# Performance work log

Hardware: AMD Instinct MI355X
Metric: run time of the kernel (lower is better)

## Reference

```python
import jax, jax.numpy as jnp
import numpy as np

INPUT_SIZE = 2048
H1 = 256
H2 = 64
NB = 8
BATCH = 16384


def setup_inputs() -> dict:
    key = jax.random.key(0)
    ks = jax.random.split(key, 8)
    x = jax.random.normal(ks[0], (BATCH, INPUT_SIZE), dtype=jnp.float32)
    bucket_indices = jax.random.randint(ks[1], (BATCH,), 0, NB, dtype=jnp.int32)
    # torch nn.Linear weights: (out_features, in_features), bias: (out_features,)
    def lin(k, fan_in, fan_out):
        kw, kb = jax.random.split(k)
        bound = 1.0 / np.sqrt(fan_in)
        W = jax.random.uniform(kw, (fan_out, fan_in), jnp.float32, -bound, bound)
        b = jax.random.uniform(kb, (fan_out,), jnp.float32, -bound, bound)
        return W, b
    W1, b1 = lin(ks[2], INPUT_SIZE, H1 * NB)
    W2, b2 = lin(ks[3], H1, H2 * NB)
    W3, b3 = lin(ks[4], H2, 1 * NB)
    return {"x": x, "bucket_indices": bucket_indices,
            "W1": W1, "b1": b1, "W2": W2, "b2": b2, "W3": W3, "b3": b3}


def _gather_bucket(all_out, idx, width):
    # all_out: (B, NB*width) -> select per-sample bucket slice -> (B, width)
    B = all_out.shape[0]
    per = all_out.reshape(B, NB, width)
    return jnp.take_along_axis(per, idx[:, None, None], axis=1)[:, 0, :]


def reference(x, bucket_indices, W1, b1, W2, b2, W3, b3):
    idx = bucket_indices.astype(jnp.int32)
    h1_all = x @ W1.T + b1                      # (B, H1*NB)
    h1 = jnp.clip(_gather_bucket(h1_all, idx, H1), 0.0, 1.0)
    h2_all = h1 @ W2.T + b2                     # (B, H2*NB)
    h2 = jnp.clip(_gather_bucket(h2_all, idx, H2), 0.0, 1.0)
    out_all = h2 @ W3.T + b3                    # (B, NB)
    out = _gather_bucket(out_all, idx, 1)       # (B, 1)
    return out[:, :, None]                      # (B, 1, 1) matches unsqueeze(-1)
```

## Files before the change

### kernel.cpp

```cpp
#include <hip/hip_runtime.h>

#define INSZ   2048
#define NH1    256
#define NH2    64
#define NB     8
#define BATCH  16384

#define TS        32
#define MAXTILES  (BATCH / TS)
#define GRIDX     (NB * MAXTILES)

#define W1F_U4   (NB * 64 * 16 * 64)
#define W2F_U4   (NB * 8 * 4 * 64)

#define META_OFF  0
#define ORDER_OFF 1024
#define W1F_OFF   (1024 + BATCH * 4)
#define W2F_OFF   (W1F_OFF + W1F_U4 * 16)
#define WS_NEED   (W2F_OFF + W2F_U4 * 16)

typedef float f4  __attribute__((ext_vector_type(4)));
typedef float f32x4 __attribute__((ext_vector_type(4)));
typedef short bf16x8 __attribute__((ext_vector_type(8)));

__device__ __forceinline__ unsigned short f2bf(float f) {
    unsigned u = __float_as_uint(f);
    u += 0x7fffu + ((u >> 16) & 1u);
    return (unsigned short)(u >> 16);
}
__device__ __forceinline__ float clamp01(float v) { return fminf(fmaxf(v, 0.0f), 1.0f); }
__device__ __forceinline__ unsigned pack2(float a, float b) {
    return (unsigned)f2bf(a) | ((unsigned)f2bf(b) << 16);
}
__device__ __forceinline__ bf16x8 mk8(uint2 lo, uint2 hi) {
    union { unsigned u[4]; bf16x8 v; } r;
    r.u[0] = lo.x; r.u[1] = lo.y; r.u[2] = hi.x; r.u[3] = hi.y;
    return r.v;
}


__global__ void k_countscan(const int* __restrict__ idx, int* __restrict__ meta) {
    __shared__ int scnt[NB];
    int t = threadIdx.x;
    if (t < NB) scnt[t] = 0;
    __syncthreads();
    int local[NB];
#pragma unroll
    for (int bb = 0; bb < NB; bb++) local[bb] = 0;
    for (int i = t; i < BATCH; i += 1024) {
        int b = idx[i];
#pragma unroll
        for (int bb = 0; bb < NB; bb++) local[bb] += (b == bb) ? 1 : 0;
    }
#pragma unroll
    for (int bb = 0; bb < NB; bb++) {
        int v = local[bb];
        v += __shfl_xor(v, 1);  v += __shfl_xor(v, 2);  v += __shfl_xor(v, 4);
        v += __shfl_xor(v, 8);  v += __shfl_xor(v, 16); v += __shfl_xor(v, 32);
        if ((t & 63) == 0) atomicAdd(&scnt[bb], v);
    }
    __syncthreads();
    if (t == 0) {
        int run = 0;
        for (int b = 0; b < NB; b++) {
            int c = scnt[b];
            meta[b]      = c;
            meta[8 + b]  = run;
            meta[16 + b] = run;
            run += c;
        }
    }
}

__global__ void k_scatter(const int* __restrict__ idx, int* __restrict__ meta,
                          int* __restrict__ order) {
    __shared__ int wcnt[16][NB];
    __shared__ int sbase[NB];
    int t = threadIdx.x;
    int i = blockIdx.x * 1024 + t;
    int b = idx[i];
    int wv = t >> 6, lane = t & 63;
    unsigned long long mymask = 0;
#pragma unroll
    for (int bb = 0; bb < NB; bb++) {
        unsigned long long m = __ballot(b == bb);
        if (b == bb) mymask = m;
        if (lane == bb) wcnt[wv][bb] = (int)__popcll(m);
    }
    int myrank = (int)__popcll(mymask & ((1ull << lane) - 1ull));
    __syncthreads();
    if (t < NB) {
        int sum = 0;
        for (int w2 = 0; w2 < 16; w2++) { int c = wcnt[w2][t]; wcnt[w2][t] = sum; sum += c; }
        sbase[t] = atomicAdd(&meta[16 + t], sum);
    }
    __syncthreads();
    order[sbase[b] + wcnt[wv][b] + myrank] = i;
}

__global__ void k_pack(const float* __restrict__ W1, const float* __restrict__ W2,
                       uint4* __restrict__ W1f, uint4* __restrict__ W2f) {
    int u = blockIdx.x * 256 + threadIdx.x;
    if (u < W1F_U4) {
        int k8 = u & 255, row = (u >> 8) & 255, bkt = u >> 16;
        int kb = k8 >> 2, quad = k8 & 3;
        int cb = row >> 4, l15 = row & 15;
        const float* p = W1 + ((size_t)(bkt * NH1 + row)) * INSZ + k8 * 8;
        f4 lo = *(const f4*)p, hi = *(const f4*)(p + 4);
        uint4 o;
        o.x = pack2(lo[0], lo[1]); o.y = pack2(lo[2], lo[3]);
        o.z = pack2(hi[0], hi[1]); o.w = pack2(hi[2], hi[3]);
        W1f[((bkt * 64 + kb) * 16 + cb) * 64 + quad * 16 + l15] = o;
    } else {
        int v = u - W1F_U4;
        if (v >= W2F_U4) return;
        int k8 = v & 31, row = (v >> 5) & 63, bkt = v >> 11;
        int kb2 = k8 >> 2, quad = k8 & 3;
        int cg2 = row >> 4, l15 = row & 15;
        const float* p = W2 + ((size_t)(bkt * NH2 + row)) * NH1 + k8 * 8;
        f4 lo = *(const f4*)p, hi = *(const f4*)(p + 4);
        uint4 o;
        o.x = pack2(lo[0], lo[1]); o.y = pack2(lo[2], lo[3]);
        o.z = pack2(hi[0], hi[1]); o.w = pack2(hi[2], hi[3]);
        W2f[((bkt * 8 + kb2) * 4 + cg2) * 64 + quad * 16 + l15] = o;
    }
}


#define MFMA16 __builtin_amdgcn_mfma_f32_16x16x32_bf16

__global__ __launch_bounds__(512, 2) void fused_v13(
    const float* __restrict__ x, const int* __restrict__ meta,
    const int* __restrict__ order,
    const short* __restrict__ W1f, const short* __restrict__ W2f,
    const float* __restrict__ b1, const float* __restrict__ b2,
    const float* __restrict__ W3, const float* __restrict__ b3,
    float* __restrict__ out)
{
    const int bkt  = blockIdx.x & 7;
    const int tile = blockIdx.x >> 3;
    const int cnt  = meta[bkt];
    const int base = tile * TS;
    if (base >= cnt) return;
    const int off = meta[8 + bkt];

    __shared__ short sX[16 * 1152];
    __shared__ short sh1[TS * 264];
    __shared__ float sPart[4][TS];

    const int t = threadIdx.x;
    const int lane = t & 63, w = t >> 6;
    const int l15 = lane & 15, quad = lane >> 4;

    const int xr = t >> 4, c16 = t & 15;
    int ir = base + xr; if (ir > cnt - 1) ir = cnt - 1;
    const float* xrow = x + (size_t)order[off + ir] * INSZ;

    const short* wp = W1f + ((size_t)bkt << 19) + (size_t)(2 * w) * 512 + lane * 8;

    f32x4 acc[2][2];
#pragma unroll
    for (int f = 0; f < 2; f++)
#pragma unroll
        for (int j = 0; j < 2; j++) acc[f][j] = (f32x4)0.0f;

#pragma unroll 1
    for (int s = 0; s < 4; s++) {
        if (s) __syncthreads();
#pragma unroll
        for (int j = 0; j < 8; j++) {
            const int col = s * 512 + c16 * 4 + j * 64;
            f4 v = *(const f4*)(xrow + col);
            const int kbL = (col >> 5) & 15, ko = col & 31;
            uint2 pk; pk.x = pack2(v[0], v[1]); pk.y = pack2(v[2], v[3]);
            *(uint2*)&sX[kbL * 1152 + xr * 36 + ko] = pk;
        }
        __syncthreads();

#pragma unroll
        for (int kbL = 0; kbL < 16; kbL++) {
            const int kb = s * 16 + kbL;
            const int ab = kbL * 1152 + l15 * 36 + quad * 8;
            uint2 lo0 = *(const uint2*)&sX[ab];
            uint2 hi0 = *(const uint2*)&sX[ab + 4];
            uint2 lo1 = *(const uint2*)&sX[ab + 576];
            uint2 hi1 = *(const uint2*)&sX[ab + 580];
            bf16x8 a0 = mk8(lo0, hi0);
            bf16x8 a1 = mk8(lo1, hi1);
            bf16x8 w0 = *(const bf16x8*)(wp + (size_t)kb * 8192);
            bf16x8 w1 = *(const bf16x8*)(wp + (size_t)kb * 8192 + 512);
            acc[0][0] = MFMA16(a0, w0, acc[0][0], 0, 0, 0);
            acc[0][1] = MFMA16(a0, w1, acc[0][1], 0, 0, 0);
            acc[1][0] = MFMA16(a1, w0, acc[1][0], 0, 0, 0);
            acc[1][1] = MFMA16(a1, w1, acc[1][1], 0, 0, 0);
        }
    }

#pragma unroll
    for (int j = 0; j < 2; j++) {
        int col = w * 32 + j * 16 + l15;
        float bias = b1[bkt * NH1 + col];
#pragma unroll
        for (int f = 0; f < 2; f++)
#pragma unroll
            for (int r = 0; r < 4; r++) {
                int row = f * 16 + quad * 4 + r;
                sh1[row * 264 + col] = (short)f2bf(clamp01(acc[f][j][r] + bias));
            }
    }
    __syncthreads();

    const int rw = w & 1, cg2 = w >> 1;
    f32x4 c2 = (f32x4)0.0f;
    const short* w2p = W2f + (size_t)bkt * 16384 + lane * 8;
#pragma unroll
    for (int kb2 = 0; kb2 < 8; kb2++) {
        bf16x8 a2 = *(const bf16x8*)&sh1[(rw * 16 + l15) * 264 + kb2 * 32 + quad * 8];
        bf16x8 bw = *(const bf16x8*)(w2p + (kb2 * 4 + cg2) * 512);
        c2 = MFMA16(a2, bw, c2, 0, 0, 0);
    }

    {
        int n2 = cg2 * 16 + l15;
        float bias2 = b2[bkt * NH2 + n2];
        float w3v   = W3[bkt * NH2 + n2];
        float sacc[4];
#pragma unroll
        for (int r = 0; r < 4; r++)
            sacc[r] = clamp01(c2[r] + bias2) * w3v;
#pragma unroll
        for (int r = 0; r < 4; r++) {
            float pp = sacc[r];
            pp += __shfl_xor(pp, 1); pp += __shfl_xor(pp, 2);
            pp += __shfl_xor(pp, 4); pp += __shfl_xor(pp, 8);
            if (l15 == 0) sPart[cg2][rw * 16 + quad * 4 + r] = pp;
        }
    }
    __syncthreads();
    if (t < TS && base + t < cnt)
        out[order[off + base + t]] =
            sPart[0][t] + sPart[1][t] + sPart[2][t] + sPart[3][t] + b3[bkt];
}


__global__ void naive_mlp(const float* __restrict__ x, const int* __restrict__ idx,
                          const float* __restrict__ W1, const float* __restrict__ b1,
                          const float* __restrict__ W2, const float* __restrict__ b2,
                          const float* __restrict__ W3, const float* __restrict__ b3,
                          float* __restrict__ out)
{
    int i = blockIdx.x;
    int b = idx[i];
    __shared__ float sx[INSZ];
    __shared__ float sh1n[NH1];
    __shared__ float sh2n[NH2];
    for (int t = threadIdx.x; t < INSZ; t += 256) sx[t] = x[(size_t)i * INSZ + t];
    __syncthreads();
    int j = threadIdx.x;
    {
        const float* wr = W1 + (size_t)(b * NH1 + j) * INSZ;
        float acc = b1[b * NH1 + j];
        for (int k = 0; k < INSZ; k++) acc += sx[k] * wr[k];
        sh1n[j] = fminf(fmaxf(acc, 0.f), 1.f);
    }
    __syncthreads();
    if (j < NH2) {
        const float* wr = W2 + (size_t)(b * NH2 + j) * NH1;
        float acc = b2[b * NH2 + j];
        for (int k = 0; k < NH1; k++) acc += sh1n[k] * wr[k];
        sh2n[j] = fminf(fmaxf(acc, 0.f), 1.f);
    }
    __syncthreads();
    if (j == 0) {
        float acc = b3[b];
        for (int k = 0; k < NH2; k++) acc += sh2n[k] * W3[b * NH2 + k];
        out[i] = acc;
    }
}

extern "C" void kernel_launch(void* const* d_in, const int* in_sizes, int n_in,
                              void* d_out, int out_size, void* d_ws, size_t ws_size,
                              hipStream_t stream) {
    const float* x  = (const float*)d_in[0];
    const int* bidx = (const int*)d_in[1];
    const float* W1 = (const float*)d_in[2];
    const float* b1 = (const float*)d_in[3];
    const float* W2 = (const float*)d_in[4];
    const float* b2 = (const float*)d_in[5];
    const float* W3 = (const float*)d_in[6];
    const float* b3 = (const float*)d_in[7];
    float* out = (float*)d_out;

    if (ws_size >= (size_t)WS_NEED) {
        char* ws = (char*)d_ws;
        int*   meta  = (int*)(ws + META_OFF);
        int*   order = (int*)(ws + ORDER_OFF);
        uint4* W1f   = (uint4*)(ws + W1F_OFF);
        uint4* W2f   = (uint4*)(ws + W2F_OFF);

        k_countscan<<<1, 1024, 0, stream>>>(bidx, meta);
        k_scatter<<<BATCH / 1024, 1024, 0, stream>>>(bidx, meta, order);
        k_pack<<<(W1F_U4 + W2F_U4) / 256, 256, 0, stream>>>(W1, W2, W1f, W2f);
        fused_v13<<<GRIDX, 512, 0, stream>>>(x, meta, order,
                                             (const short*)W1f, (const short*)W2f,
                                             b1, b2, W3, b3, out);
    } else {
        naive_mlp<<<BATCH, 256, 0, stream>>>(x, bidx, W1, b1, W2, b2, W3, b3, out);
    }
}
```

Measured before the change: 275.3 us.

## Load x directly into MFMA registers, drop LDS staging, halve row tile

Shrinks the per-block row tile from 32 to 16 samples and the block from 512 to 256 threads. Each lane now reads its x fragment straight from global memory and converts it to bf16 in registers, so the shared-memory staging buffer and its barriers are gone. Each wave now computes 64 hidden columns for all 16 rows instead of 32 columns for 32 rows. The cost is that W1 is reused across only 16 rows, which doubles W1 traffic per sample, and the x reads are less coalesced (8 floats per lane per row).

Measured after the change: 333.0 us. 1.21x slower.

```diff
diff --git a/kernel.cpp b/kernel.cpp
--- a/kernel.cpp
+++ b/kernel.cpp
@@ -6,7 +6,7 @@
 #define NB     8
 #define BATCH  16384
 
-#define TS        32
+#define TS        16
 #define MAXTILES  (BATCH / TS)
 #define GRIDX     (NB * MAXTILES)
 
@@ -31,11 +31,6 @@
 __device__ __forceinline__ float clamp01(float v) { return fminf(fmaxf(v, 0.0f), 1.0f); }
 __device__ __forceinline__ unsigned pack2(float a, float b) {
     return (unsigned)f2bf(a) | ((unsigned)f2bf(b) << 16);
-}
-__device__ __forceinline__ bf16x8 mk8(uint2 lo, uint2 hi) {
-    union { unsigned u[4]; bf16x8 v; } r;
-    r.u[0] = lo.x; r.u[1] = lo.y; r.u[2] = hi.x; r.u[3] = hi.y;
-    return r.v;
 }
 
 
@@ -129,7 +124,7 @@
 
 #define MFMA16 __builtin_amdgcn_mfma_f32_16x16x32_bf16
 
-__global__ __launch_bounds__(512, 2) void fused_v13(
+__global__ __launch_bounds__(256, 4) void fused_v14(
     const float* __restrict__ x, const int* __restrict__ meta,
     const int* __restrict__ order,
     const short* __restrict__ W1f, const short* __restrict__ W2f,
@@ -144,7 +139,6 @@
     if (base >= cnt) return;
     const int off = meta[8 + bkt];
 
-    __shared__ short sX[16 * 1152];
     __shared__ short sh1[TS * 264];
     __shared__ float sPart[4][TS];
 
@@ -152,88 +146,65 @@
     const int lane = t & 63, w = t >> 6;
     const int l15 = lane & 15, quad = lane >> 4;
 
-    const int xr = t >> 4, c16 = t & 15;
-    int ir = base + xr; if (ir > cnt - 1) ir = cnt - 1;
-    const float* xrow = x + (size_t)order[off + ir] * INSZ;
-
-    const short* wp = W1f + ((size_t)bkt << 19) + (size_t)(2 * w) * 512 + lane * 8;
-
-    f32x4 acc[2][2];
-#pragma unroll
-    for (int f = 0; f < 2; f++)
-#pragma unroll
-        for (int j = 0; j < 2; j++) acc[f][j] = (f32x4)0.0f;
-
-#pragma unroll 1
-    for (int s = 0; s < 4; s++) {
-        if (s) __syncthreads();
-#pragma unroll
-        for (int j = 0; j < 8; j++) {
-            const int col = s * 512 + c16 * 4 + j * 64;
-            f4 v = *(const f4*)(xrow + col);
-            const int kbL = (col >> 5) & 15, ko = col & 31;
-            uint2 pk; pk.x = pack2(v[0], v[1]); pk.y = pack2(v[2], v[3]);
-            *(uint2*)&sX[kbL * 1152 + xr * 36 + ko] = pk;
+    int ir = base + l15; if (ir > cnt - 1) ir = cnt - 1;
+    const float* xg = x + (size_t)order[off + ir] * INSZ + quad * 8;
+
+    const short* wp = W1f + ((size_t)bkt << 19) + (size_t)(4 * w) * 512 + lane * 8;
+
+    f32x4 acc[4];
+#pragma unroll
+    for (int i = 0; i < 4; i++) acc[i] = (f32x4)0.0f;
+
+#pragma unroll 2
+    for (int kb = 0; kb < 64; kb++) {
+        f4 lo = *(const f4*)(xg + kb * 32);
+        f4 hi = *(const f4*)(xg + kb * 32 + 4);
+        const short* wq = wp + (size_t)kb * 8192;
+        bf16x8 w0 = *(const bf16x8*)(wq);
+        bf16x8 w1 = *(const bf16x8*)(wq + 512);
+        bf16x8 w2 = *(const bf16x8*)(wq + 1024);
+        bf16x8 w3r = *(const bf16x8*)(wq + 1536);
+        uint4 u;
+        u.x = pack2(lo[0], lo[1]); u.y = pack2(lo[2], lo[3]);
+        u.z = pack2(hi[0], hi[1]); u.w = pack2(hi[2], hi[3]);
+        bf16x8 a = *(bf16x8*)&u;
+        acc[0] = MFMA16(a, w0, acc[0], 0, 0, 0);
+        acc[1] = MFMA16(a, w1, acc[1], 0, 0, 0);
+        acc[2] = MFMA16(a, w2, acc[2], 0, 0, 0);
+        acc[3] = MFMA16(a, w3r, acc[3], 0, 0, 0);
+    }
+
+#pragma unroll
+    for (int i = 0; i < 4; i++) {
+        int col = w * 64 + i * 16 + l15;
+        float bias = b1[bkt * NH1 + col];
+#pragma unroll
+        for (int r = 0; r < 4; r++) {
+            int row = quad * 4 + r;
+            sh1[row * 264 + col] = (short)f2bf(clamp01(acc[i][r] + bias));
         }
-        __syncthreads();
-
-#pragma unroll
-        for (int kbL = 0; kbL < 16; kbL++) {
-            const int kb = s * 16 + kbL;
-            const int ab = kbL * 1152 + l15 * 36 + quad * 8;
-            uint2 lo0 = *(const uint2*)&sX[ab];
-            uint2 hi0 = *(const uint2*)&sX[ab + 4];
-            uint2 lo1 = *(const uint2*)&sX[ab + 576];
-            uint2 hi1 = *(const uint2*)&sX[ab + 580];
-            bf16x8 a0 = mk8(lo0, hi0);
-            bf16x8 a1 = mk8(lo1, hi1);
-            bf16x8 w0 = *(const bf16x8*)(wp + (size_t)kb * 8192);
-            bf16x8 w1 = *(const bf16x8*)(wp + (size_t)kb * 8192 + 512);
-            acc[0][0] = MFMA16(a0, w0, acc[0][0], 0, 0, 0);
-            acc[0][1] = MFMA16(a0, w1, acc[0][1], 0, 0, 0);
-            acc[1][0] = MFMA16(a1, w0, acc[1][0], 0, 0, 0);
-            acc[1][1] = MFMA16(a1, w1, acc[1][1], 0, 0, 0);
-        }
-    }
-
-#pragma unroll
-    for (int j = 0; j < 2; j++) {
-        int col = w * 32 + j * 16 + l15;
-        float bias = b1[bkt * NH1 + col];
-#pragma unroll
-        for (int f = 0; f < 2; f++)
-#pragma unroll
-            for (int r = 0; r < 4; r++) {
-                int row = f * 16 + quad * 4 + r;
-                sh1[row * 264 + col] = (short)f2bf(clamp01(acc[f][j][r] + bias));
-            }
-    }
-    __syncthreads();
-
-    const int rw = w & 1, cg2 = w >> 1;
+    }
+    __syncthreads();
+
     f32x4 c2 = (f32x4)0.0f;
     const short* w2p = W2f + (size_t)bkt * 16384 + lane * 8;
 #pragma unroll
     for (int kb2 = 0; kb2 < 8; kb2++) {
-        bf16x8 a2 = *(const bf16x8*)&sh1[(rw * 16 + l15) * 264 + kb2 * 32 + quad * 8];
-        bf16x8 bw = *(const bf16x8*)(w2p + (kb2 * 4 + cg2) * 512);
+        bf16x8 a2 = *(const bf16x8*)&sh1[l15 * 264 + kb2 * 32 + quad * 8];
+        bf16x8 bw = *(const bf16x8*)(w2p + (kb2 * 4 + w) * 512);
         c2 = MFMA16(a2, bw, c2, 0, 0, 0);
     }
 
     {
-        int n2 = cg2 * 16 + l15;
+        int n2 = w * 16 + l15;
         float bias2 = b2[bkt * NH2 + n2];
         float w3v   = W3[bkt * NH2 + n2];
-        float sacc[4];
-#pragma unroll
-        for (int r = 0; r < 4; r++)
-            sacc[r] = clamp01(c2[r] + bias2) * w3v;
 #pragma unroll
         for (int r = 0; r < 4; r++) {
-            float pp = sacc[r];
+            float pp = clamp01(c2[r] + bias2) * w3v;
             pp += __shfl_xor(pp, 1); pp += __shfl_xor(pp, 2);
             pp += __shfl_xor(pp, 4); pp += __shfl_xor(pp, 8);
-            if (l15 == 0) sPart[cg2][rw * 16 + quad * 4 + r] = pp;
+            if (l15 == 0) sPart[w][quad * 4 + r] = pp;
         }
     }
     __syncthreads();
@@ -301,7 +272,7 @@
         k_countscan<<<1, 1024, 0, stream>>>(bidx, meta);
         k_scatter<<<BATCH / 1024, 1024, 0, stream>>>(bidx, meta, order);
         k_pack<<<(W1F_U4 + W2F_U4) / 256, 256, 0, stream>>>(W1, W2, W1f, W2f);
-        fused_v13<<<GRIDX, 512, 0, stream>>>(x, meta, order,
+        fused_v14<<<GRIDX, 256, 0, stream>>>(x, meta, order,
                                              (const short*)W1f, (const short*)W2f,
                                              b1, b2, W3, b3, out);
     } else {
```
